# Kernel optimization log

Measured on AMD Instinct MI355X. Metric: run time of the kernel, lower is better.

## Reference

```python
import jax, jax.numpy as jnp
import numpy as np

D_MODEL = 1024
NUM_HEADS = 16
HEAD_DIM = D_MODEL // NUM_HEADS
B, L = 2, 2048


def setup_inputs() -> dict:
    key = jax.random.key(0)
    ks = jax.random.split(key, 9)
    s = 0.02
    return {
        "query": jax.random.normal(ks[0], (B, L, D_MODEL), dtype=jnp.float32),
        "key": jax.random.normal(ks[1], (B, L, D_MODEL), dtype=jnp.float32),
        "value": jax.random.normal(ks[2], (B, L, D_MODEL), dtype=jnp.float32),
        "mask": jax.random.randint(ks[3], (B, L), 0, 2, dtype=jnp.int32),
        "Wq": jax.random.normal(ks[4], (D_MODEL, D_MODEL), dtype=jnp.float32) * s,
        "Wk": jax.random.normal(ks[5], (D_MODEL, D_MODEL), dtype=jnp.float32) * s,
        "Wv": jax.random.normal(ks[6], (D_MODEL, D_MODEL), dtype=jnp.float32) * s,
        "Wo": jax.random.normal(ks[7], (D_MODEL, D_MODEL), dtype=jnp.float32) * s,
        "bo": jnp.zeros((D_MODEL,), dtype=jnp.float32),
    }


def _split_heads(x):
    # (B, L, d_model) -> (B, H, L, head_dim)
    b, l, _ = x.shape
    return x.reshape(b, l, NUM_HEADS, HEAD_DIM).transpose(0, 2, 1, 3)


def reference(query, key, value, mask, Wq, Wk, Wv, Wo, bo):
    # nn.Linear(bias=False): x @ W.T
    q = _split_heads(query @ Wq.T)   # (B, H, L, hd)
    k = _split_heads(key @ Wk.T)
    v = _split_heads(value @ Wv.T)

    scores = jnp.einsum("bhqd,bhkd->bhqk", q, k) / jnp.sqrt(jnp.float32(HEAD_DIM))
    # padding mask over keys: (B, L) -> (B, 1, 1, L); 0 = pad -> -inf
    keep = (mask[:, None, None, :] != 0)
    scores = jnp.where(keep, scores, -jnp.inf)

    attn = jax.nn.softmax(scores, axis=-1)
    # original zeroes NaN rows (fully-masked query rows)
    attn = jnp.where(jnp.isnan(attn), jnp.zeros_like(attn), attn)
    # dropout is identity in eval/reference mode

    ctx = jnp.einsum("bhqk,bhkd->bhqd", attn, v)           # (B, H, L, hd)
    ctx = ctx.transpose(0, 2, 1, 3).reshape(B, L, D_MODEL)  # combine heads
    return ctx @ Wo.T + bo
```

## Files before the change

### kernel.cpp

```cpp
#include <hip/hip_runtime.h>

typedef unsigned short u16;
typedef __bf16 bf16x8 __attribute__((ext_vector_type(8)));
typedef __bf16 bf16x4 __attribute__((ext_vector_type(4)));
typedef float floatx4 __attribute__((ext_vector_type(4)));
typedef u16 u16x4 __attribute__((ext_vector_type(4)));
typedef unsigned uint32x2 __attribute__((ext_vector_type(2)));
typedef unsigned uint32x4 __attribute__((ext_vector_type(4)));

#define MEG ((size_t)(1u << 20))

__device__ __forceinline__ u16 f2bf(float f) {
  unsigned int u = __float_as_uint(f);
  u += 0x7fffu + ((u >> 16) & 1u);
  return (u16)(u >> 16);
}

__device__ __forceinline__ unsigned cvt_pk_bf16(float lo, float hi) {
  unsigned r;
  asm("v_cvt_pk_bf16_f32 %0, %1, %2" : "=v"(r) : "v"(lo), "v"(hi));
  return r;
}

__device__ __forceinline__ void load_lds16(const u16* g, u16* l) {
  __builtin_amdgcn_global_load_lds((const __attribute__((address_space(1))) unsigned int*)g,
                                   (__attribute__((address_space(3))) unsigned int*)l,
                                   16, 0, 0);
}

__global__ __launch_bounds__(256) void cvt7(
    const float* __restrict__ s0, const float* __restrict__ s1,
    const float* __restrict__ s2, const float* __restrict__ s3,
    const float* __restrict__ s4, const float* __restrict__ s5,
    const float* __restrict__ s6, u16* __restrict__ dst)
{
  size_t e = ((size_t)blockIdx.x * 256 + threadIdx.x) * 16;
  unsigned m = (unsigned)(e >> 20);
  const float* s; size_t off;
  if (m < 4)       { s = s0; off = e; }
  else if (m < 8)  { s = s1; off = e - 4 * MEG; }
  else if (m < 12) { s = s2; off = e - 8 * MEG; }
  else if (m < 13) { s = s3; off = e - 12 * MEG; }
  else if (m < 14) { s = s4; off = e - 13 * MEG; }
  else if (m < 15) { s = s5; off = e - 14 * MEG; }
  else             { s = s6; off = e - 15 * MEG; }
  float4 f[4];
#pragma unroll
  for (int t = 0; t < 4; ++t)
    f[t] = *reinterpret_cast<const float4*>(s + off + t * 4);
#pragma unroll
  for (int t = 0; t < 4; ++t) {
    u16x4 o;
    o.x = f2bf(f[t].x); o.y = f2bf(f[t].y); o.z = f2bf(f[t].z); o.w = f2bf(f[t].w);
    *reinterpret_cast<u16x4*>(dst + e + t * 4) = o;
  }
}

__global__ __launch_bounds__(256) void gemm_proj(
    const u16* __restrict__ Abase, const u16* __restrict__ Bbase,
    u16* __restrict__ Cbase, u16* __restrict__ VtB,
    int K, long zA, long zB, long zC)
{
  __shared__ __align__(16) u16 As[128 * 64];
  __shared__ __align__(16) u16 Bs[128 * 64];
  const int tid = threadIdx.x;
  const int w = tid >> 6, ln = tid & 63;
  const int lm = ln & 15, lq = ln >> 4;
  const int wm = w >> 1, wn = w & 1;
  const long m0 = (long)blockIdx.x * 128, n0 = (long)blockIdx.y * 128;
  const u16* A = Abase + (size_t)blockIdx.z * (size_t)zA;
  const u16* B = Bbase + (size_t)blockIdx.z * (size_t)zB;

  const int r0 = tid >> 3;
  const int kc = (tid & 7) ^ (r0 & 7);
  const u16* gA = A + (m0 + r0) * (long)K + kc * 8;
  const u16* gB = B + (n0 + r0) * (long)K + kc * 8;
  const long rstep = 32L * K;

  const int sl0 = (lq ^ (lm & 7)) * 8;
  const int sl1 = ((4 + lq) ^ (lm & 7)) * 8;
  const u16* ab0 = &As[(wm * 64 + lm) * 64 + sl0];
  const u16* ab1 = &As[(wm * 64 + lm) * 64 + sl1];
  const u16* bb0 = &Bs[(wn * 64 + lm) * 64 + sl0];
  const u16* bb1 = &Bs[(wn * 64 + lm) * 64 + sl1];

  const floatx4 z4 = {0.f, 0.f, 0.f, 0.f};
  floatx4 acc[4][4];
#pragma unroll
  for (int i = 0; i < 4; ++i)
#pragma unroll
    for (int j = 0; j < 4; ++j) acc[i][j] = z4;

  for (int k0 = 0; k0 < K; k0 += 64) {
#pragma unroll
    for (int t = 0; t < 4; ++t) {
      load_lds16(gA + t * rstep, &As[(t * 256 + w * 64) * 8]);
      load_lds16(gB + t * rstep, &Bs[(t * 256 + w * 64) * 8]);
    }
    gA += 64; gB += 64;
    __syncthreads();
    bf16x8 af[4][2], bfr[4][2];
#pragma unroll
    for (int i = 0; i < 4; ++i) {
      af[i][0] = *reinterpret_cast<const bf16x8*>(ab0 + i * 1024);
      af[i][1] = *reinterpret_cast<const bf16x8*>(ab1 + i * 1024);
    }
#pragma unroll
    for (int j = 0; j < 4; ++j) {
      bfr[j][0] = *reinterpret_cast<const bf16x8*>(bb0 + j * 1024);
      bfr[j][1] = *reinterpret_cast<const bf16x8*>(bb1 + j * 1024);
    }
#pragma unroll
    for (int i = 0; i < 4; ++i)
#pragma unroll
      for (int j = 0; j < 4; ++j) {
        acc[i][j] = __builtin_amdgcn_mfma_f32_16x16x32_bf16(af[i][0], bfr[j][0], acc[i][j], 0, 0, 0);
        acc[i][j] = __builtin_amdgcn_mfma_f32_16x16x32_bf16(af[i][1], bfr[j][1], acc[i][j], 0, 0, 0);
      }
    __syncthreads();
  }

  if (blockIdx.z == 2) {
#pragma unroll
    for (int i = 0; i < 4; ++i) {
      long row = m0 + wm * 64 + i * 16 + lq * 4;
      int bq = (int)(row >> 11);
      int l  = (int)(row & 2047);
#pragma unroll
      for (int j = 0; j < 4; ++j) {
        long col = n0 + wn * 64 + j * 16 + lm;
        int hh = (int)(col >> 6), dd = (int)(col & 63);
        u16x4 o;
        o.x = f2bf(acc[i][j][0]); o.y = f2bf(acc[i][j][1]);
        o.z = f2bf(acc[i][j][2]); o.w = f2bf(acc[i][j][3]);
        *reinterpret_cast<u16x4*>(&VtB[((size_t)(bq * 16 + hh)) * 131072 +
                                       (size_t)dd * 2048 + l]) = o;
      }
    }
    return;
  }

#pragma unroll
  for (int i = 0; i < 4; ++i) {
    long row = m0 + wm * 64 + i * 16 + lq * 4;
#pragma unroll
    for (int j = 0; j < 4; ++j) {
      long col = n0 + wn * 64 + j * 16 + lm;
#pragma unroll
      for (int r = 0; r < 4; ++r) {
        size_t idx = (size_t)(row + r) * 1024 + (size_t)col;
        (Cbase + (size_t)blockIdx.z * (size_t)zC)[idx] = f2bf(acc[i][j][r]);
      }
    }
  }
}

__global__ __launch_bounds__(256) void gemm_out_fused(
    const u16* __restrict__ OpA, const u16* __restrict__ OpB,
    const float* __restrict__ psA, const float* __restrict__ psB,
    const u16* __restrict__ Wo, const float* __restrict__ bias,
    float* __restrict__ Cout)
{
  __shared__ __align__(16) u16 As[64 * 64];
  __shared__ __align__(16) u16 Bs[128 * 64];
  const int tid = threadIdx.x;
  const int w = tid >> 6, ln = tid & 63;
  const int lm = ln & 15, lq = ln >> 4;
  const int wm = w >> 1, wn = w & 1;
  const long m0 = (long)blockIdx.x * 64, n0 = (long)blockIdx.y * 128;

  const int r0 = tid >> 3;
  const int kc = (tid & 7) ^ (r0 & 7);
  const u16* gB = Wo + (n0 + r0) * 1024 + kc * 8;
  const long rstep = 32L * 1024;

  const int sl0 = (lq ^ (lm & 7)) * 8;
  const int sl1 = ((4 + lq) ^ (lm & 7)) * 8;
  const u16* ab0 = &As[(wm * 32 + lm) * 64 + sl0];
  const u16* ab1 = &As[(wm * 32 + lm) * 64 + sl1];
  const u16* bb0 = &Bs[(wn * 64 + lm) * 64 + sl0];
  const u16* bb1 = &Bs[(wn * 64 + lm) * 64 + sl1];

  int rowg[2]; int qlb[2];
#pragma unroll
  for (int t = 0; t < 2; ++t) {
    rowg[t] = (int)m0 + r0 + t * 32;
    int b = rowg[t] >> 11, l = rowg[t] & 2047;
    qlb[t] = (b << 4) * 2048 + l;
  }

  const floatx4 z4 = {0.f, 0.f, 0.f, 0.f};
  floatx4 acc[2][4];
#pragma unroll
  for (int i = 0; i < 2; ++i)
#pragma unroll
    for (int j = 0; j < 4; ++j) acc[i][j] = z4;

  for (int k0 = 0; k0 < 1024; k0 += 64) {
#pragma unroll
    for (int t = 0; t < 4; ++t)
      load_lds16(gB + t * rstep, &Bs[(t * 256 + w * 64) * 8]);
    gB += 64;
    const int h = k0 >> 6;
#pragma unroll
    for (int t = 0; t < 2; ++t) {
      int ql = qlb[t] + h * 2048;
      float s = psA[ql] + psB[ql];
      float inv = (s > 0.f) ? __builtin_amdgcn_rcpf(s) : 0.f;
      size_t idx = (size_t)rowg[t] * 1024 + k0 + kc * 8;
      uint4 ua = *reinterpret_cast<const uint4*>(OpA + idx);
      uint4 ub = *reinterpret_cast<const uint4*>(OpB + idx);
      uint4 uo;
      const unsigned* pa = reinterpret_cast<const unsigned*>(&ua);
      const unsigned* pb = reinterpret_cast<const unsigned*>(&ub);
      unsigned* po = reinterpret_cast<unsigned*>(&uo);
#pragma unroll
      for (int i = 0; i < 4; ++i) {
        float alo = __uint_as_float(pa[i] << 16);
        float ahi = __uint_as_float(pa[i] & 0xFFFF0000u);
        float blo = __uint_as_float(pb[i] << 16);
        float bhi = __uint_as_float(pb[i] & 0xFFFF0000u);
        float olo = (alo + blo) * inv;
        float ohi = (ahi + bhi) * inv;
        po[i] = (unsigned)f2bf(olo) | ((unsigned)f2bf(ohi) << 16);
      }
      *reinterpret_cast<uint4*>(&As[(size_t)(t * 256 + tid) * 8]) = uo;
    }
    __syncthreads();
    bf16x8 af[2][2], bfr[4][2];
#pragma unroll
    for (int i = 0; i < 2; ++i) {
      af[i][0] = *reinterpret_cast<const bf16x8*>(ab0 + i * 1024);
      af[i][1] = *reinterpret_cast<const bf16x8*>(ab1 + i * 1024);
    }
#pragma unroll
    for (int j = 0; j < 4; ++j) {
      bfr[j][0] = *reinterpret_cast<const bf16x8*>(bb0 + j * 1024);
      bfr[j][1] = *reinterpret_cast<const bf16x8*>(bb1 + j * 1024);
    }
#pragma unroll
    for (int i = 0; i < 2; ++i)
#pragma unroll
      for (int j = 0; j < 4; ++j) {
        acc[i][j] = __builtin_amdgcn_mfma_f32_16x16x32_bf16(af[i][0], bfr[j][0], acc[i][j], 0, 0, 0);
        acc[i][j] = __builtin_amdgcn_mfma_f32_16x16x32_bf16(af[i][1], bfr[j][1], acc[i][j], 0, 0, 0);
      }
    __syncthreads();
  }

#pragma unroll
  for (int i = 0; i < 2; ++i) {
    long row = m0 + wm * 32 + i * 16 + lq * 4;
#pragma unroll
    for (int j = 0; j < 4; ++j) {
      long col = n0 + wn * 64 + j * 16 + lm;
      float bv = bias[col];
#pragma unroll
      for (int r = 0; r < 4; ++r)
        Cout[(size_t)(row + r) * 1024 + (size_t)col] = acc[i][j][r] + bv;
    }
  }
}

__global__ __launch_bounds__(256, 4) void attn_kernel(
    const u16* __restrict__ Qp, const u16* __restrict__ Kp,
    const u16* __restrict__ Vt, const int* __restrict__ mask,
    u16* __restrict__ OpBase, float* __restrict__ psAB)
{
  __shared__ __align__(16) u16 Ks[2 * 64 * 64];
  __shared__ __align__(16) u16 Vts[2 * 64 * 64];
  __shared__ __align__(16) float mball[1024];

  const int tid = threadIdx.x;
  const int w = tid >> 6, ln = tid & 63;
  const int lm = ln & 15, lq = ln >> 4;
  const int bh = blockIdx.y, b = bh >> 4, h = bh & 15;
  const int q0 = blockIdx.x * 128;
  const int kz = blockIdx.z;

  const u16* Qh = Qp + (size_t)b * 2048 * 1024 + h * 64;
  const u16* Kh = Kp + (size_t)b * 2048 * 1024 + (size_t)kz * 1024 * 1024 + h * 64;
  const u16* Vth = Vt + (size_t)bh * 64 * 2048 + kz * 1024;
  u16* Op = OpBase + (size_t)kz * 8 * MEG;
  float* psZ = psAB + (size_t)kz * 65536;

  const int* mrowp = mask + b * 2048 + kz * 1024;
#pragma unroll
  for (int t = 0; t < 4; ++t) {
    int i = t * 256 + tid;
    mball[i] = (mrowp[i] != 0) ? 0.f : -__builtin_inff();
  }

  bf16x8 qf[2][2];
#pragma unroll
  for (int m = 0; m < 2; ++m) {
    int qrow = q0 + w * 32 + m * 16 + lm;
    qf[m][0] = *reinterpret_cast<const bf16x8*>(Qh + (size_t)qrow * 1024 + lq * 8);
    qf[m][1] = *reinterpret_cast<const bf16x8*>(Qh + (size_t)qrow * 1024 + 32 + lq * 8);
  }

  const int sl0 = (lq ^ (lm & 7)) * 8;
  const int sl1 = ((4 + lq) ^ (lm & 7)) * 8;
  const u16* kb0 = &Ks[lm * 64 + sl0];
  const u16* kb1 = &Ks[lm * 64 + sl1];
  const u16* vb0 = &Vts[lm * 64 + sl0];
  const u16* vb1 = &Vts[lm * 64 + sl1];
  const float* mbi = mball + lq * 4;

  const int r0 = tid >> 3;
  const int kc = (tid & 7) ^ (r0 & 7);
  const u16* gK0 = Kh + (size_t)r0 * 1024 + kc * 8;
  const u16* gK1 = gK0 + 32 * 1024;
  const u16* gV0 = Vth + (size_t)r0 * 2048 + kc * 8;
  const u16* gV1 = gV0 + 32 * 2048;

  const floatx4 z4 = {0.f, 0.f, 0.f, 0.f};
  floatx4 O[2][4];
#pragma unroll
  for (int m = 0; m < 2; ++m)
#pragma unroll
    for (int j = 0; j < 4; ++j) O[m][j] = z4;
  float psum[2] = {0.f, 0.f};
  const float SCL = 0.18033688011112042f;

  load_lds16(gK0, &Ks[(w * 64) * 8]);
  load_lds16(gK1, &Ks[(256 + w * 64) * 8]);
  load_lds16(gV0, &Vts[(w * 64) * 8]);
  load_lds16(gV1, &Vts[(256 + w * 64) * 8]);
  gK0 += 64 * 1024; gK1 += 64 * 1024; gV0 += 64; gV1 += 64;
  __syncthreads();

  for (int it = 0; it < 16; ++it) {
    const int cur = it & 1;
    if (it < 15) {
      const int nx = (cur ^ 1) * 4096;
      load_lds16(gK0, &Ks[nx + (w * 64) * 8]);
      load_lds16(gK1, &Ks[nx + (256 + w * 64) * 8]);
      load_lds16(gV0, &Vts[nx + (w * 64) * 8]);
      load_lds16(gV1, &Vts[nx + (256 + w * 64) * 8]);
      gK0 += 64 * 1024; gK1 += 64 * 1024; gV0 += 64; gV1 += 64;
    }
    const int bofs = cur * 4096;

#pragma unroll
    for (int m = 0; m < 2; ++m) {
#pragma unroll
      for (int h2 = 0; h2 < 2; ++h2) {
        floatx4 S0, S1;
        {
          bf16x8 k00 = *reinterpret_cast<const bf16x8*>(kb0 + bofs + (2 * h2) * 1024);
          bf16x8 k01 = *reinterpret_cast<const bf16x8*>(kb1 + bofs + (2 * h2) * 1024);
          bf16x8 k10 = *reinterpret_cast<const bf16x8*>(kb0 + bofs + (2 * h2 + 1) * 1024);
          bf16x8 k11 = *reinterpret_cast<const bf16x8*>(kb1 + bofs + (2 * h2 + 1) * 1024);
          __builtin_amdgcn_s_setprio(1);
          S0 = __builtin_amdgcn_mfma_f32_16x16x32_bf16(k00, qf[m][0], z4, 0, 0, 0);
          S0 = __builtin_amdgcn_mfma_f32_16x16x32_bf16(k01, qf[m][1], S0, 0, 0, 0);
          S1 = __builtin_amdgcn_mfma_f32_16x16x32_bf16(k10, qf[m][0], z4, 0, 0, 0);
          S1 = __builtin_amdgcn_mfma_f32_16x16x32_bf16(k11, qf[m][1], S1, 0, 0, 0);
          __builtin_amdgcn_s_setprio(0);
        }

        float4 mbA = *reinterpret_cast<const float4*>(mbi + (2 * h2) * 16);
        float4 mbB = *reinterpret_cast<const float4*>(mbi + (2 * h2 + 1) * 16);
        float a0 = __builtin_amdgcn_exp2f(fmaf(S0[0], SCL, mbA.x));
        float a1 = __builtin_amdgcn_exp2f(fmaf(S0[1], SCL, mbA.y));
        float a2 = __builtin_amdgcn_exp2f(fmaf(S0[2], SCL, mbA.z));
        float a3 = __builtin_amdgcn_exp2f(fmaf(S0[3], SCL, mbA.w));
        psum[m] += (a0 + a1) + (a2 + a3);
        unsigned c00 = cvt_pk_bf16(a0, a1);
        unsigned c01 = cvt_pk_bf16(a2, a3);
        float b0 = __builtin_amdgcn_exp2f(fmaf(S1[0], SCL, mbB.x));
        float b1 = __builtin_amdgcn_exp2f(fmaf(S1[1], SCL, mbB.y));
        float b2 = __builtin_amdgcn_exp2f(fmaf(S1[2], SCL, mbB.z));
        float b3 = __builtin_amdgcn_exp2f(fmaf(S1[3], SCL, mbB.w));
        psum[m] += (b0 + b1) + (b2 + b3);
        unsigned c10 = cvt_pk_bf16(b0, b1);
        unsigned c11 = cvt_pk_bf16(b2, b3);

        uint32x2 t1a = __builtin_amdgcn_permlane32_swap(c00, c10, false, false);
        uint32x2 t2a = __builtin_amdgcn_permlane16_swap(t1a.x, t1a.y, false, false);
        uint32x2 t1b = __builtin_amdgcn_permlane32_swap(c01, c11, false, false);
        uint32x2 t2b = __builtin_amdgcn_permlane16_swap(t1b.x, t1b.y, false, false);
        uint32x4 wv = {t2a.x, t2b.x, t2a.y, t2b.y};
        bf16x8 pf = __builtin_bit_cast(bf16x8, wv);

        const u16* vb = (h2 ? vb1 : vb0) + bofs;
        __builtin_amdgcn_s_setprio(1);
#pragma unroll
        for (int j = 0; j < 4; ++j) {
          bf16x8 vfj = *reinterpret_cast<const bf16x8*>(vb + j * 1024);
          O[m][j] = __builtin_amdgcn_mfma_f32_16x16x32_bf16(pf, vfj, O[m][j], 0, 0, 0);
        }
        __builtin_amdgcn_s_setprio(0);
      }
    }
    mbi += 64;
    __syncthreads();
  }

#pragma unroll
  for (int m = 0; m < 2; ++m) {
    float s = psum[m];
    s += __shfl_xor(s, 16, 64);
    s += __shfl_xor(s, 32, 64);
    int prow = q0 + w * 32 + m * 16 + lm;
    if (lq == 0) psZ[bh * 2048 + prow] = s;
#pragma unroll
    for (int r = 0; r < 4; ++r) {
      int row = q0 + w * 32 + m * 16 + lq * 4 + r;
      size_t base = ((size_t)b * 2048 + row) * 1024 + h * 64 + lm;
#pragma unroll
      for (int j = 0; j < 4; ++j)
        Op[base + j * 16] = f2bf(O[m][j][r]);
    }
  }
}

extern "C" void kernel_launch(void* const* d_in, const int* in_sizes, int n_in,
                              void* d_out, int out_size, void* d_ws, size_t ws_size,
                              hipStream_t stream) {
  const float* q  = (const float*)d_in[0];
  const float* k  = (const float*)d_in[1];
  const float* v  = (const float*)d_in[2];
  const int*   mk = (const int*)  d_in[3];
  const float* wq = (const float*)d_in[4];
  const float* wk = (const float*)d_in[5];
  const float* wv = (const float*)d_in[6];
  const float* wo = (const float*)d_in[7];
  const float* bo = (const float*)d_in[8];

  u16* ws16 = (u16*)d_ws;
  u16* Xq  = ws16;
  u16* Wq  = ws16 + 12 * MEG;
  u16* Wo  = ws16 + 15 * MEG;
  u16* Qp  = ws16 + 16 * MEG;
  u16* Kp  = ws16 + 20 * MEG;
  u16* Vt  = ws16 + 24 * MEG;
  u16* OpA = ws16;
  u16* OpB = ws16 + 8 * MEG;
  float* psAB = (float*)(ws16 + 12 * MEG);

  cvt7<<<dim3(4096), dim3(256), 0, stream>>>(q, k, v, wq, wk, wv, wo, ws16);

  gemm_proj<<<dim3(32, 8, 3), dim3(256), 0, stream>>>(
      Xq, Wq, Qp, Vt, 1024, (long)(4 * MEG), (long)MEG, (long)(4 * MEG));

  attn_kernel<<<dim3(16, 32, 2), dim3(256), 0, stream>>>(Qp, Kp, Vt, mk, OpA, psAB);

  gemm_out_fused<<<dim3(64, 8), dim3(256), 0, stream>>>(
      OpA, OpB, psAB, psAB + 65536, Wo, bo, (float*)d_out);
}
```

Before: 214.7 us.

## Drop LDS mask buffer, remap blocks across XCDs, raise attention occupancy

The per-block shared-memory mask array is removed. Each iteration now loads the 64 mask ints straight from global memory into registers and converts them to additive biases. The block index is remapped so that blocks sharing the same head and key-split land on the same XCD, improving L2 reuse of K/V. Launch bounds rise to 5 waves per SIMD to raise occupancy, at the risk of register pressure or spills and extra global mask loads in the inner loop.

```diff
diff --git a/kernel.cpp b/kernel.cpp
--- a/kernel.cpp
+++ b/kernel.cpp
@@ -262,21 +262,25 @@
   }
 }
 
-__global__ __launch_bounds__(256, 4) void attn_kernel(
+__global__ __launch_bounds__(256, 5) void attn_kernel(
     const u16* __restrict__ Qp, const u16* __restrict__ Kp,
     const u16* __restrict__ Vt, const int* __restrict__ mask,
     u16* __restrict__ OpBase, float* __restrict__ psAB)
 {
   __shared__ __align__(16) u16 Ks[2 * 64 * 64];
   __shared__ __align__(16) u16 Vts[2 * 64 * 64];
-  __shared__ __align__(16) float mball[1024];
 
   const int tid = threadIdx.x;
   const int w = tid >> 6, ln = tid & 63;
   const int lm = ln & 15, lq = ln >> 4;
-  const int bh = blockIdx.y, b = bh >> 4, h = bh & 15;
-  const int q0 = blockIdx.x * 128;
-  const int kz = blockIdx.z;
+
+  const int lid = blockIdx.x + (blockIdx.y << 4) + (blockIdx.z << 9);
+  const int xcd = lid & 7, slot = lid >> 3;
+  const int group = (xcd << 3) + (slot >> 4);
+  const int qt = slot & 15;
+  const int kz = group & 1;
+  const int bh = group >> 1, b = bh >> 4, h = bh & 15;
+  const int q0 = qt * 128;
 
   const u16* Qh = Qp + (size_t)b * 2048 * 1024 + h * 64;
   const u16* Kh = Kp + (size_t)b * 2048 * 1024 + (size_t)kz * 1024 * 1024 + h * 64;
@@ -284,12 +288,7 @@
   u16* Op = OpBase + (size_t)kz * 8 * MEG;
   float* psZ = psAB + (size_t)kz * 65536;
 
-  const int* mrowp = mask + b * 2048 + kz * 1024;
-#pragma unroll
-  for (int t = 0; t < 4; ++t) {
-    int i = t * 256 + tid;
-    mball[i] = (mrowp[i] != 0) ? 0.f : -__builtin_inff();
-  }
+  const int* gM = mask + b * 2048 + kz * 1024 + lq * 4;
 
   bf16x8 qf[2][2];
 #pragma unroll
@@ -305,7 +304,6 @@
   const u16* kb1 = &Ks[lm * 64 + sl1];
   const u16* vb0 = &Vts[lm * 64 + sl0];
   const u16* vb1 = &Vts[lm * 64 + sl1];
-  const float* mbi = mball + lq * 4;
 
   const int r0 = tid >> 3;
   const int kc = (tid & 7) ^ (r0 & 7);
@@ -322,6 +320,7 @@
     for (int j = 0; j < 4; ++j) O[m][j] = z4;
   float psum[2] = {0.f, 0.f};
   const float SCL = 0.18033688011112042f;
+  const float NINF = -__builtin_inff();
 
   load_lds16(gK0, &Ks[(w * 64) * 8]);
   load_lds16(gK1, &Ks[(256 + w * 64) * 8]);
@@ -341,6 +340,17 @@
       gK0 += 64 * 1024; gK1 += 64 * 1024; gV0 += 64; gV1 += 64;
     }
     const int bofs = cur * 4096;
+
+    float4 mb4[4];
+#pragma unroll
+    for (int n = 0; n < 4; ++n) {
+      int4 mi = *reinterpret_cast<const int4*>(gM + n * 16);
+      mb4[n].x = mi.x ? 0.f : NINF;
+      mb4[n].y = mi.y ? 0.f : NINF;
+      mb4[n].z = mi.z ? 0.f : NINF;
+      mb4[n].w = mi.w ? 0.f : NINF;
+    }
+    gM += 64;
 
 #pragma unroll
     for (int m = 0; m < 2; ++m) {
@@ -360,8 +370,8 @@
           __builtin_amdgcn_s_setprio(0);
         }
 
-        float4 mbA = *reinterpret_cast<const float4*>(mbi + (2 * h2) * 16);
-        float4 mbB = *reinterpret_cast<const float4*>(mbi + (2 * h2 + 1) * 16);
+        float4 mbA = mb4[2 * h2];
+        float4 mbB = mb4[2 * h2 + 1];
         float a0 = __builtin_amdgcn_exp2f(fmaf(S0[0], SCL, mbA.x));
         float a1 = __builtin_amdgcn_exp2f(fmaf(S0[1], SCL, mbA.y));
         float a2 = __builtin_amdgcn_exp2f(fmaf(S0[2], SCL, mbA.z));
@@ -394,7 +404,6 @@
         __builtin_amdgcn_s_setprio(0);
       }
     }
-    mbi += 64;
     __syncthreads();
   }
 
```

New measurement: 246.3 us. +14.7%, slower.

## Swizzle attention block mapping across XCDs and share K/V fragments across query sub-tiles

Applied to the files above, without the earlier changes.

Remaps the linear block id so that all query tiles of one (batch, head, key-half) group land on the same XCD, improving L2 reuse of K/V tiles. It also reorders the inner loop so each K and V LDS fragment is loaded once and used for both 16-row query sub-tiles, halving LDS reads and giving the MFMA unit more independent work. The trade-off is more live registers (two score tiles and two P fragments at once), which may pressure occupancy under the 256x4 launch bound.

```diff
diff --git a/kernel.cpp b/kernel.cpp
--- a/kernel.cpp
+++ b/kernel.cpp
@@ -274,9 +274,14 @@
   const int tid = threadIdx.x;
   const int w = tid >> 6, ln = tid & 63;
   const int lm = ln & 15, lq = ln >> 4;
-  const int bh = blockIdx.y, b = bh >> 4, h = bh & 15;
-  const int q0 = blockIdx.x * 128;
-  const int kz = blockIdx.z;
+
+  const int lid = blockIdx.x + (blockIdx.y << 4) + (blockIdx.z << 9);
+  const int xcd = lid & 7, slot = lid >> 3;
+  const int group = (xcd << 3) + (slot >> 4);
+  const int qt = slot & 15;
+  const int kz = group & 1;
+  const int bh = group >> 1, b = bh >> 4, h = bh & 15;
+  const int q0 = qt * 128;
 
   const u16* Qh = Qp + (size_t)b * 2048 * 1024 + h * 64;
   const u16* Kh = Kp + (size_t)b * 2048 * 1024 + (size_t)kz * 1024 * 1024 + h * 64;
@@ -342,37 +347,47 @@
     }
     const int bofs = cur * 4096;
 
-#pragma unroll
-    for (int m = 0; m < 2; ++m) {
-#pragma unroll
-      for (int h2 = 0; h2 < 2; ++h2) {
-        floatx4 S0, S1;
-        {
-          bf16x8 k00 = *reinterpret_cast<const bf16x8*>(kb0 + bofs + (2 * h2) * 1024);
-          bf16x8 k01 = *reinterpret_cast<const bf16x8*>(kb1 + bofs + (2 * h2) * 1024);
-          bf16x8 k10 = *reinterpret_cast<const bf16x8*>(kb0 + bofs + (2 * h2 + 1) * 1024);
-          bf16x8 k11 = *reinterpret_cast<const bf16x8*>(kb1 + bofs + (2 * h2 + 1) * 1024);
-          __builtin_amdgcn_s_setprio(1);
-          S0 = __builtin_amdgcn_mfma_f32_16x16x32_bf16(k00, qf[m][0], z4, 0, 0, 0);
-          S0 = __builtin_amdgcn_mfma_f32_16x16x32_bf16(k01, qf[m][1], S0, 0, 0, 0);
-          S1 = __builtin_amdgcn_mfma_f32_16x16x32_bf16(k10, qf[m][0], z4, 0, 0, 0);
-          S1 = __builtin_amdgcn_mfma_f32_16x16x32_bf16(k11, qf[m][1], S1, 0, 0, 0);
-          __builtin_amdgcn_s_setprio(0);
+    float4 mb4[4];
+#pragma unroll
+    for (int n = 0; n < 4; ++n)
+      mb4[n] = *reinterpret_cast<const float4*>(mbi + n * 16);
+    mbi += 64;
+
+#pragma unroll
+    for (int h2 = 0; h2 < 2; ++h2) {
+      floatx4 S[2][2];
+      {
+        bf16x8 k00 = *reinterpret_cast<const bf16x8*>(kb0 + bofs + (2 * h2) * 1024);
+        bf16x8 k01 = *reinterpret_cast<const bf16x8*>(kb1 + bofs + (2 * h2) * 1024);
+        bf16x8 k10 = *reinterpret_cast<const bf16x8*>(kb0 + bofs + (2 * h2 + 1) * 1024);
+        bf16x8 k11 = *reinterpret_cast<const bf16x8*>(kb1 + bofs + (2 * h2 + 1) * 1024);
+        __builtin_amdgcn_s_setprio(1);
+#pragma unroll
+        for (int m = 0; m < 2; ++m) {
+          S[m][0] = __builtin_amdgcn_mfma_f32_16x16x32_bf16(k00, qf[m][0], z4, 0, 0, 0);
+          S[m][0] = __builtin_amdgcn_mfma_f32_16x16x32_bf16(k01, qf[m][1], S[m][0], 0, 0, 0);
+          S[m][1] = __builtin_amdgcn_mfma_f32_16x16x32_bf16(k10, qf[m][0], z4, 0, 0, 0);
+          S[m][1] = __builtin_amdgcn_mfma_f32_16x16x32_bf16(k11, qf[m][1], S[m][1], 0, 0, 0);
         }
-
-        float4 mbA = *reinterpret_cast<const float4*>(mbi + (2 * h2) * 16);
-        float4 mbB = *reinterpret_cast<const float4*>(mbi + (2 * h2 + 1) * 16);
-        float a0 = __builtin_amdgcn_exp2f(fmaf(S0[0], SCL, mbA.x));
-        float a1 = __builtin_amdgcn_exp2f(fmaf(S0[1], SCL, mbA.y));
-        float a2 = __builtin_amdgcn_exp2f(fmaf(S0[2], SCL, mbA.z));
-        float a3 = __builtin_amdgcn_exp2f(fmaf(S0[3], SCL, mbA.w));
+        __builtin_amdgcn_s_setprio(0);
+      }
+
+      float4 mbA = mb4[2 * h2];
+      float4 mbB = mb4[2 * h2 + 1];
+      bf16x8 pf[2];
+#pragma unroll
+      for (int m = 0; m < 2; ++m) {
+        float a0 = __builtin_amdgcn_exp2f(fmaf(S[m][0][0], SCL, mbA.x));
+        float a1 = __builtin_amdgcn_exp2f(fmaf(S[m][0][1], SCL, mbA.y));
+        float a2 = __builtin_amdgcn_exp2f(fmaf(S[m][0][2], SCL, mbA.z));
+        float a3 = __builtin_amdgcn_exp2f(fmaf(S[m][0][3], SCL, mbA.w));
         psum[m] += (a0 + a1) + (a2 + a3);
         unsigned c00 = cvt_pk_bf16(a0, a1);
         unsigned c01 = cvt_pk_bf16(a2, a3);
-        float b0 = __builtin_amdgcn_exp2f(fmaf(S1[0], SCL, mbB.x));
-        float b1 = __builtin_amdgcn_exp2f(fmaf(S1[1], SCL, mbB.y));
-        float b2 = __builtin_amdgcn_exp2f(fmaf(S1[2], SCL, mbB.z));
-        float b3 = __builtin_amdgcn_exp2f(fmaf(S1[3], SCL, mbB.w));
+        float b0 = __builtin_amdgcn_exp2f(fmaf(S[m][1][0], SCL, mbB.x));
+        float b1 = __builtin_amdgcn_exp2f(fmaf(S[m][1][1], SCL, mbB.y));
+        float b2 = __builtin_amdgcn_exp2f(fmaf(S[m][1][2], SCL, mbB.z));
+        float b3 = __builtin_amdgcn_exp2f(fmaf(S[m][1][3], SCL, mbB.w));
         psum[m] += (b0 + b1) + (b2 + b3);
         unsigned c10 = cvt_pk_bf16(b0, b1);
         unsigned c11 = cvt_pk_bf16(b2, b3);
@@ -382,19 +397,19 @@
         uint32x2 t1b = __builtin_amdgcn_permlane32_swap(c01, c11, false, false);
         uint32x2 t2b = __builtin_amdgcn_permlane16_swap(t1b.x, t1b.y, false, false);
         uint32x4 wv = {t2a.x, t2b.x, t2a.y, t2b.y};
-        bf16x8 pf = __builtin_bit_cast(bf16x8, wv);
-
-        const u16* vb = (h2 ? vb1 : vb0) + bofs;
-        __builtin_amdgcn_s_setprio(1);
-#pragma unroll
-        for (int j = 0; j < 4; ++j) {
-          bf16x8 vfj = *reinterpret_cast<const bf16x8*>(vb + j * 1024);
-          O[m][j] = __builtin_amdgcn_mfma_f32_16x16x32_bf16(pf, vfj, O[m][j], 0, 0, 0);
-        }
-        __builtin_amdgcn_s_setprio(0);
-      }
-    }
-    mbi += 64;
+        pf[m] = __builtin_bit_cast(bf16x8, wv);
+      }
+
+      const u16* vb = (h2 ? vb1 : vb0) + bofs;
+      __builtin_amdgcn_s_setprio(1);
+#pragma unroll
+      for (int j = 0; j < 4; ++j) {
+        bf16x8 vfj = *reinterpret_cast<const bf16x8*>(vb + j * 1024);
+        O[0][j] = __builtin_amdgcn_mfma_f32_16x16x32_bf16(pf[0], vfj, O[0][j], 0, 0, 0);
+        O[1][j] = __builtin_amdgcn_mfma_f32_16x16x32_bf16(pf[1], vfj, O[1][j], 0, 0, 0);
+      }
+      __builtin_amdgcn_s_setprio(0);
+    }
     __syncthreads();
   }
 
```

Result: slower. 219.2 us (+2.1%).
